# Optimization experiments

Hardware: AMD Instinct MI355X
Metric: run time of the kernel (lower is better)

The kernel has to match this reference:

```python
import jax, jax.numpy as jnp
import numpy as np

N = 50000   # nodes
E = 1600000 # edges
D = 64      # feature dim


def gcn_conv(x, edge_index, W, b):
    """PyG GCNConv: x' = D^-1/2 (A+I) D^-1/2 (x W) + b."""
    n = x.shape[0]
    xw = x @ W                                   # [N, D_out] linear first (PyG order)
    loop = jnp.arange(n)
    src = jnp.concatenate([edge_index[0], loop])  # add self-loops
    dst = jnp.concatenate([edge_index[1], loop])
    deg = jax.ops.segment_sum(jnp.ones_like(src, dtype=xw.dtype), dst, num_segments=n)
    dinv = jnp.where(deg > 0, jax.lax.rsqrt(deg), 0.0)
    norm = dinv[src] * dinv[dst]                  # symmetric normalization
    out = jax.ops.segment_sum(norm[:, None] * xw[src], dst, num_segments=n)
    return out + b


def setup_inputs() -> dict:
    key = jax.random.key(0)
    k1, k2, k3, k4 = jax.random.split(key, 4)
    x = jax.random.normal(k1, (N, D), dtype=jnp.float32)
    edge_index = jax.random.randint(k2, (2, E), 0, N, dtype=jnp.int64)
    s = 1.0 / np.sqrt(D)
    W1 = jax.random.normal(k3, (D, D), dtype=jnp.float32) * s
    b1 = jnp.zeros((D,), dtype=jnp.float32)
    W2 = jax.random.normal(k4, (D, D), dtype=jnp.float32) * s
    b2 = jnp.zeros((D,), dtype=jnp.float32)
    return {"x": x, "edge_index": edge_index, "W1": W1, "b1": b1, "W2": W2, "b2": b2}


def reference(x, edge_index, W1, b1, W2, b2):
    h = gcn_conv(x, edge_index, W1, b1)
    h = jax.nn.relu(h)  # dropout is identity in eval mode
    out = gcn_conv(h, edge_index, W2, b2)
    return out
```

## Files before the change

### kernel.cpp

```cpp
#include <hip/hip_runtime.h>
#include <hip/hip_fp16.h>


#define P1_EDGES 4096
#define BSTRIDE 16384

typedef float vfloat4 __attribute__((ext_vector_type(4)));

__global__ void bucket_gemm_kernel(const int* __restrict__ src, const int* __restrict__ dst,
                                   unsigned* __restrict__ cursor, unsigned* __restrict__ ebuf,
                                   const float4* __restrict__ X4, const float* __restrict__ W,
                                   __half* __restrict__ Yh,
                                   int e, int B, int n, int nbP1) {
    __shared__ unsigned hist[256];
    __shared__ unsigned base[256];
    __shared__ float4 Ws[64][16];
    int bid = blockIdx.x;
    if (bid < nbP1) {
        for (int i = threadIdx.x; i < B; i += 1024) hist[i] = 0;
        __syncthreads();
        int e0 = bid * P1_EDGES;
        int tbase = e0 + (int)threadIdx.x * 4;
        int4 sv = make_int4(0, 0, 0, 0), dv = make_int4(0, 0, 0, 0);
        if (tbase + 3 < e) {
            sv = ((const int4*)(src + e0))[threadIdx.x];
            dv = ((const int4*)(dst + e0))[threadIdx.x];
        } else {
            if (tbase + 0 < e) { sv.x = src[tbase + 0]; dv.x = dst[tbase + 0]; }
            if (tbase + 1 < e) { sv.y = src[tbase + 1]; dv.y = dst[tbase + 1]; }
            if (tbase + 2 < e) { sv.z = src[tbase + 2]; dv.z = dst[tbase + 2]; }
        }
        unsigned bk[4], rk[4], pk[4];
        bool vk[4];
#pragma unroll
        for (int k = 0; k < 4; ++k) {
            int t = tbase + k;
            vk[k] = (t < e);
            bk[k] = 0; rk[k] = 0; pk[k] = 0;
            if (vk[k]) {
                unsigned s = (unsigned)(k == 0 ? sv.x : k == 1 ? sv.y : k == 2 ? sv.z : sv.w);
                unsigned d = (unsigned)(k == 0 ? dv.x : k == 1 ? dv.y : k == 2 ? dv.z : dv.w);
                unsigned b = d >> 8;
                bk[k] = b;
                rk[k] = atomicAdd(&hist[b], 1u);
                pk[k] = (d << 16) | s;
            }
        }
        __syncthreads();
        for (int i = threadIdx.x; i < B; i += 1024)
            base[i] = hist[i] ? atomicAdd(&cursor[i], hist[i]) : 0u;
        __syncthreads();
#pragma unroll
        for (int k = 0; k < 4; ++k)
            if (vk[k]) {
                unsigned slot = base[bk[k]] + rk[k];
                if (slot < (unsigned)BSTRIDE)
                    ebuf[(size_t)bk[k] * BSTRIDE + slot] = pk[k];
            }
    } else {
        for (int i = threadIdx.x; i < 64 * 16; i += 1024)
            Ws[i >> 4][i & 15] = ((const float4*)W)[i];
        __syncthreads();
        int lane = threadIdx.x & 63;
        int l = lane & 15;
        int gbase = lane & 48;
        int wid = (bid - nbP1) * 16 + (threadIdx.x >> 6);
        int row = wid * 4 + (lane >> 4);
        if (row >= n) return;
        float4 xv = X4[(size_t)row * 16 + l];
        float4 acc = make_float4(0.f, 0.f, 0.f, 0.f);
#pragma unroll
        for (int k = 0; k < 64; ++k) {
            float comp = (k & 3) == 0 ? xv.x : (k & 3) == 1 ? xv.y : (k & 3) == 2 ? xv.z : xv.w;
            float a = __shfl(comp, gbase + (k >> 2));
            float4 w = Ws[k][l];
            acc.x = fmaf(a, w.x, acc.x); acc.y = fmaf(a, w.y, acc.y);
            acc.z = fmaf(a, w.z, acc.z); acc.w = fmaf(a, w.w, acc.w);
        }
        __half2 h0 = __floats2half2_rn(acc.x, acc.y);
        __half2 h1 = __floats2half2_rn(acc.z, acc.w);
        uint2 o;
        o.x = *(const unsigned*)&h0;
        o.y = *(const unsigned*)&h1;
        *(uint2*)(Yh + (size_t)row * 64 + 4 * l) = o;
    }
}

__global__ void statsfill_kernel(const unsigned* __restrict__ ebuf,
                                 const unsigned* __restrict__ bcnt,
                                 unsigned* __restrict__ rpf,
                                 __half* __restrict__ xwh1,
                                 unsigned short* __restrict__ csr, int n, int e) {
    __shared__ unsigned pos[256];
    __shared__ unsigned sh[256];
    __shared__ unsigned rpl[256];
    __shared__ float dl[256];
    __shared__ unsigned bs;
    int b = blockIdx.x;
    int w0 = b << 8;
    int wlen = min(w0 + 256, n) - w0;
    unsigned c0 = 0;
    if (threadIdx.x < 256) { c0 = bcnt[threadIdx.x]; sh[threadIdx.x] = c0; }
    __syncthreads();
    for (int off = 1; off < 256; off <<= 1) {
        unsigned t = 0;
        if (threadIdx.x < 256 && threadIdx.x >= (unsigned)off) t = sh[threadIdx.x - off];
        __syncthreads();
        if (threadIdx.x < 256) sh[threadIdx.x] += t;
        __syncthreads();
    }
    if (threadIdx.x == (unsigned)b) bs = sh[b] - c0;
    if (threadIdx.x < 256) pos[threadIdx.x] = 0;
    __syncthreads();
    unsigned cnt = bcnt[b];
    const unsigned* eb = ebuf + (size_t)b * BSTRIDE;
    for (unsigned j = threadIdx.x; j < cnt; j += 1024)
        atomicAdd(&pos[(eb[j] >> 16) - w0], 1u);
    __syncthreads();
    unsigned v = 0;
    if (threadIdx.x < 256) { v = pos[threadIdx.x]; sh[threadIdx.x] = v; }
    __syncthreads();
    for (int off = 1; off < 256; off <<= 1) {
        unsigned t = 0;
        if (threadIdx.x < 256 && threadIdx.x >= (unsigned)off) t = sh[threadIdx.x - off];
        __syncthreads();
        if (threadIdx.x < 256) sh[threadIdx.x] += t;
        __syncthreads();
    }
    if (threadIdx.x < 256) {
        unsigned rp = bs + sh[threadIdx.x] - v;
        rpl[threadIdx.x] = rp;
        dl[threadIdx.x] = rsqrtf((float)v + 1.0f);
        if ((int)threadIdx.x < wlen) rpf[w0 + threadIdx.x] = rp;
        pos[threadIdx.x] = 0;
    }
    if (b == (int)gridDim.x - 1 && threadIdx.x == 0) rpf[n] = (unsigned)e;
    __syncthreads();
    for (int i = threadIdx.x; i < (wlen << 3); i += 1024) {
        int r = i >> 3, c = i & 7;
        float di = dl[r];
        uint4* p16 = (uint4*)(xwh1 + ((size_t)(w0 + r) << 6)) + c;
        uint4 hv = *p16;
        float2 f0 = __half22float2(*(const __half2*)&hv.x);
        float2 f1 = __half22float2(*(const __half2*)&hv.y);
        float2 f2 = __half22float2(*(const __half2*)&hv.z);
        float2 f3 = __half22float2(*(const __half2*)&hv.w);
        __half2 g0 = __floats2half2_rn(f0.x * di, f0.y * di);
        __half2 g1 = __floats2half2_rn(f1.x * di, f1.y * di);
        __half2 g2 = __floats2half2_rn(f2.x * di, f2.y * di);
        __half2 g3 = __floats2half2_rn(f3.x * di, f3.y * di);
        hv.x = *(const unsigned*)&g0; hv.y = *(const unsigned*)&g1;
        hv.z = *(const unsigned*)&g2; hv.w = *(const unsigned*)&g3;
        *p16 = hv;
    }
    for (unsigned j = threadIdx.x; j < cnt; j += 1024) {
        unsigned p = eb[j];
        unsigned d = (p >> 16) - w0;
        unsigned r = atomicAdd(&pos[d], 1u);
        csr[rpl[d] + r] = (unsigned short)(p & 0xffffu);
    }
}

struct f8 { float4 a, b; };

__device__ __forceinline__ f8 aggregate_row8(const __half* __restrict__ xwh,
                                             const unsigned* __restrict__ csrw,
                                             unsigned start, unsigned end,
                                             int row, int l8, int gbase) {
    f8 acc;
    {
        uint4 hv = *(const uint4*)(xwh + (size_t)row * 64 + 8 * l8);
        float2 f0 = __half22float2(*(const __half2*)&hv.x);
        float2 f1 = __half22float2(*(const __half2*)&hv.y);
        float2 f2 = __half22float2(*(const __half2*)&hv.z);
        float2 f3 = __half22float2(*(const __half2*)&hv.w);
        acc.a = make_float4(f0.x, f0.y, f1.x, f1.y);
        acc.b = make_float4(f2.x, f2.y, f3.x, f3.y);
    }
    unsigned wb = start >> 1;
    unsigned jw = wb + (unsigned)l8;
    unsigned ed = (jw * 2 < end) ? __builtin_nontemporal_load(&csrw[jw]) : 0u;
    for (unsigned base = wb; base * 2 < end; base += 8) {
        unsigned jn = base + 8 + (unsigned)l8;
        unsigned ed_next = (jn * 2 < end) ? __builtin_nontemporal_load(&csrw[jn]) : 0u;
#pragma unroll
        for (int t = 0; t < 8; ++t) {
            unsigned p = __shfl(ed, gbase + t);
            unsigned i0 = (base + (unsigned)t) * 2;
            int s0 = (int)(p & 0xffffu);
            int s1 = (int)(p >> 16);
            float w0 = (i0 >= start && i0 < end) ? 1.0f : 0.0f;
            float w1 = (i0 + 1 < end) ? 1.0f : 0.0f;
            uint4 hv0 = *(const uint4*)(xwh + (size_t)s0 * 64 + 8 * l8);
            uint4 hv1 = *(const uint4*)(xwh + (size_t)s1 * 64 + 8 * l8);
            float2 a0 = __half22float2(*(const __half2*)&hv0.x);
            float2 a1 = __half22float2(*(const __half2*)&hv0.y);
            float2 a2 = __half22float2(*(const __half2*)&hv0.z);
            float2 a3 = __half22float2(*(const __half2*)&hv0.w);
            acc.a.x = fmaf(w0, a0.x, acc.a.x); acc.a.y = fmaf(w0, a0.y, acc.a.y);
            acc.a.z = fmaf(w0, a1.x, acc.a.z); acc.a.w = fmaf(w0, a1.y, acc.a.w);
            acc.b.x = fmaf(w0, a2.x, acc.b.x); acc.b.y = fmaf(w0, a2.y, acc.b.y);
            acc.b.z = fmaf(w0, a3.x, acc.b.z); acc.b.w = fmaf(w0, a3.y, acc.b.w);
            float2 c0 = __half22float2(*(const __half2*)&hv1.x);
            float2 c1 = __half22float2(*(const __half2*)&hv1.y);
            float2 c2 = __half22float2(*(const __half2*)&hv1.z);
            float2 c3 = __half22float2(*(const __half2*)&hv1.w);
            acc.a.x = fmaf(w1, c0.x, acc.a.x); acc.a.y = fmaf(w1, c0.y, acc.a.y);
            acc.a.z = fmaf(w1, c1.x, acc.a.z); acc.a.w = fmaf(w1, c1.y, acc.a.w);
            acc.b.x = fmaf(w1, c2.x, acc.b.x); acc.b.y = fmaf(w1, c2.y, acc.b.y);
            acc.b.z = fmaf(w1, c3.x, acc.b.z); acc.b.w = fmaf(w1, c3.y, acc.b.w);
        }
        ed = ed_next;
    }
    return acc;
}

__global__ void __launch_bounds__(256, 3)
gather_gemm_kernel(const __half* __restrict__ xwh, const unsigned* __restrict__ csrw,
                   const unsigned* __restrict__ row_ptr,
                   const float* __restrict__ b1, const float* __restrict__ W2,
                   __half* __restrict__ Yh, int n) {
    __shared__ float4 Ws[64][16];
    for (int i = threadIdx.x; i < 64 * 16; i += blockDim.x)
        Ws[i >> 4][i & 15] = ((const float4*)W2)[i];
    __syncthreads();
    int lane = threadIdx.x & 63;
    int l8 = lane & 7;
    int gbase = lane & 56;
    int wid = blockIdx.x * (blockDim.x >> 6) + (threadIdx.x >> 6);
    int row = wid * 8 + (lane >> 3);
    if (row >= n) return;
    unsigned start = row_ptr[row], end = row_ptr[row + 1];
    float di = rsqrtf((float)(end - start) + 1.0f);
    f8 acc = aggregate_row8(xwh, csrw, start, end, row, l8, gbase);
    float4 ba = ((const float4*)b1)[2 * l8];
    float4 bb = ((const float4*)b1)[2 * l8 + 1];
    float h0 = fmaxf(fmaf(di, acc.a.x, ba.x), 0.f);
    float h1 = fmaxf(fmaf(di, acc.a.y, ba.y), 0.f);
    float h2 = fmaxf(fmaf(di, acc.a.z, ba.z), 0.f);
    float h3 = fmaxf(fmaf(di, acc.a.w, ba.w), 0.f);
    float h4 = fmaxf(fmaf(di, acc.b.x, bb.x), 0.f);
    float h5 = fmaxf(fmaf(di, acc.b.y, bb.y), 0.f);
    float h6 = fmaxf(fmaf(di, acc.b.z, bb.z), 0.f);
    float h7 = fmaxf(fmaf(di, acc.b.w, bb.w), 0.f);
    float4 o0 = make_float4(0.f, 0.f, 0.f, 0.f);
    float4 o1 = make_float4(0.f, 0.f, 0.f, 0.f);
#pragma unroll
    for (int k = 0; k < 64; ++k) {
        float comp = (k & 7) == 0 ? h0 : (k & 7) == 1 ? h1 : (k & 7) == 2 ? h2 :
                     (k & 7) == 3 ? h3 : (k & 7) == 4 ? h4 : (k & 7) == 5 ? h5 :
                     (k & 7) == 6 ? h6 : h7;
        float a = __shfl(comp, gbase + (k >> 3));
        float4 w0 = Ws[k][2 * l8];
        float4 w1 = Ws[k][2 * l8 + 1];
        o0.x = fmaf(a, w0.x, o0.x); o0.y = fmaf(a, w0.y, o0.y);
        o0.z = fmaf(a, w0.z, o0.z); o0.w = fmaf(a, w0.w, o0.w);
        o1.x = fmaf(a, w1.x, o1.x); o1.y = fmaf(a, w1.y, o1.y);
        o1.z = fmaf(a, w1.z, o1.z); o1.w = fmaf(a, w1.w, o1.w);
    }
    __half2 p0 = __floats2half2_rn(o0.x * di, o0.y * di);
    __half2 p1 = __floats2half2_rn(o0.z * di, o0.w * di);
    __half2 p2 = __floats2half2_rn(o1.x * di, o1.y * di);
    __half2 p3 = __floats2half2_rn(o1.z * di, o1.w * di);
    uint4 o;
    o.x = *(const unsigned*)&p0; o.y = *(const unsigned*)&p1;
    o.z = *(const unsigned*)&p2; o.w = *(const unsigned*)&p3;
    *(uint4*)(Yh + (size_t)row * 64 + 8 * l8) = o;
}

__global__ void __launch_bounds__(256, 3)
gather_out_kernel(const __half* __restrict__ xwh, const unsigned* __restrict__ csrw,
                  const unsigned* __restrict__ row_ptr,
                  const float* __restrict__ bias, float4* __restrict__ out4, int n) {
    int lane = threadIdx.x & 63;
    int l8 = lane & 7;
    int gbase = lane & 56;
    int wid = blockIdx.x * (blockDim.x >> 6) + (threadIdx.x >> 6);
    int row = wid * 8 + (lane >> 3);
    if (row >= n) return;
    unsigned start = row_ptr[row], end = row_ptr[row + 1];
    float di = rsqrtf((float)(end - start) + 1.0f);
    f8 acc = aggregate_row8(xwh, csrw, start, end, row, l8, gbase);
    float4 ba = ((const float4*)bias)[2 * l8];
    float4 bb = ((const float4*)bias)[2 * l8 + 1];
    vfloat4 oa, ob;
    oa.x = fmaf(di, acc.a.x, ba.x); oa.y = fmaf(di, acc.a.y, ba.y);
    oa.z = fmaf(di, acc.a.z, ba.z); oa.w = fmaf(di, acc.a.w, ba.w);
    ob.x = fmaf(di, acc.b.x, bb.x); ob.y = fmaf(di, acc.b.y, bb.y);
    ob.z = fmaf(di, acc.b.z, bb.z); ob.w = fmaf(di, acc.b.w, bb.w);
    vfloat4* o4 = (vfloat4*)out4;
    __builtin_nontemporal_store(oa, &o4[(size_t)row * 16 + 2 * l8]);
    __builtin_nontemporal_store(ob, &o4[(size_t)row * 16 + 2 * l8 + 1]);
}

extern "C" void kernel_launch(void* const* d_in, const int* in_sizes, int n_in,
                              void* d_out, int out_size, void* d_ws, size_t ws_size,
                              hipStream_t stream) {
    const float* x  = (const float*)d_in[0];
    const int*   ei = (const int*)d_in[1];
    const float* W1 = (const float*)d_in[2];
    const float* b1 = (const float*)d_in[3];
    const float* W2 = (const float*)d_in[4];
    const float* b2 = (const float*)d_in[5];
    const int n = in_sizes[0] / 64;
    const int e = in_sizes[1] / 2;
    const int* src = ei;
    const int* dst = ei + e;

    char* ws = (char*)d_ws;
    size_t off = 0;
    auto alloc = [&](size_t bytes) -> void* {
        void* p = ws + off;
        off = (off + bytes + 255) & ~(size_t)255;
        return p;
    };
    unsigned* rpf    = (unsigned*)alloc((size_t)(n + 1) * 4);
    unsigned* cursor = (unsigned*)alloc(256 * 4);
    unsigned short* csr = (unsigned short*)alloc(((size_t)e / 2 + 64) * 4);
    const int B = (n + 255) / 256;
    unsigned* ebuf   = (unsigned*)alloc((size_t)B * BSTRIDE * 4);
    __half*   xwh1   = (__half*)alloc((size_t)n * 64 * 2);
    __half*   xwh2   = (__half*)alloc((size_t)n * 64 * 2);
    float*    outf   = (float*)d_out;

    const int nbP1 = (e + P1_EDGES - 1) / P1_EDGES;
    const int gblk64 = (n + 63) / 64;

    hipMemsetAsync(cursor, 0, 256 * 4, stream);
    bucket_gemm_kernel<<<nbP1 + gblk64, 1024, 0, stream>>>(
        src, dst, cursor, ebuf, (const float4*)x, W1, xwh1, e, B, n, nbP1);
    statsfill_kernel<<<B, 1024, 0, stream>>>(ebuf, cursor, rpf, xwh1, csr, n, e);

    const int gblk32 = (n + 31) / 32;

    gather_gemm_kernel<<<gblk32, 256, 0, stream>>>(xwh1, (const unsigned*)csr, rpf, b1, W2, xwh2, n);
    gather_out_kernel<<<gblk32, 256, 0, stream>>>(xwh2, (const unsigned*)csr, rpf, b2, (float4*)outf, n);
}
```

Before: 171.5 us.

## Split feature columns into two halves for cache-resident gather passes

Stores the transformed node features as two separate 32-column fp16 tables, and performs each neighbour aggregation as two passes, one per half. Each pass therefore touches a table half the size, which is meant to improve L2/LLC hit rates on the random source-row gathers. The first layer's halves are combined in the second gather kernel before the W2 matmul. In exchange, the CSR index stream is read twice per layer and there are extra kernel launches plus an intermediate hA buffer.

Result: slower. 203.0 us (+18.4%).

```diff
diff --git a/kernel.cpp b/kernel.cpp
--- a/kernel.cpp
+++ b/kernel.cpp
@@ -10,7 +10,7 @@
 __global__ void bucket_gemm_kernel(const int* __restrict__ src, const int* __restrict__ dst,
                                    unsigned* __restrict__ cursor, unsigned* __restrict__ ebuf,
                                    const float4* __restrict__ X4, const float* __restrict__ W,
-                                   __half* __restrict__ Yh,
+                                   __half* __restrict__ YA, __half* __restrict__ YB,
                                    int e, int B, int n, int nbP1) {
     __shared__ unsigned hist[256];
     __shared__ unsigned base[256];
@@ -82,14 +82,15 @@
         uint2 o;
         o.x = *(const unsigned*)&h0;
         o.y = *(const unsigned*)&h1;
-        *(uint2*)(Yh + (size_t)row * 64 + 4 * l) = o;
+        __half* dstp = (l < 8 ? YA : YB) + ((size_t)row << 5) + 4 * (l & 7);
+        *(uint2*)dstp = o;
     }
 }
 
 __global__ void statsfill_kernel(const unsigned* __restrict__ ebuf,
                                  const unsigned* __restrict__ bcnt,
                                  unsigned* __restrict__ rpf,
-                                 __half* __restrict__ xwh1,
+                                 __half* __restrict__ xwA, __half* __restrict__ xwB,
                                  unsigned short* __restrict__ csr, int n, int e) {
     __shared__ unsigned pos[256];
     __shared__ unsigned sh[256];
@@ -139,7 +140,8 @@
     for (int i = threadIdx.x; i < (wlen << 3); i += 1024) {
         int r = i >> 3, c = i & 7;
         float di = dl[r];
-        uint4* p16 = (uint4*)(xwh1 + ((size_t)(w0 + r) << 6)) + c;
+        __half* tb = (c < 4) ? xwA : xwB;
+        uint4* p16 = (uint4*)(tb + ((size_t)(w0 + r) << 5)) + (c & 3);
         uint4 hv = *p16;
         float2 f0 = __half22float2(*(const __half2*)&hv.x);
         float2 f1 = __half22float2(*(const __half2*)&hv.y);
@@ -163,13 +165,13 @@
 
 struct f8 { float4 a, b; };
 
-__device__ __forceinline__ f8 aggregate_row8(const __half* __restrict__ xwh,
+__device__ __forceinline__ f8 aggregate_half(const __half* __restrict__ xw,
                                              const unsigned* __restrict__ csrw,
                                              unsigned start, unsigned end,
-                                             int row, int l8, int gbase) {
+                                             int row, int l4, int gb) {
     f8 acc;
     {
-        uint4 hv = *(const uint4*)(xwh + (size_t)row * 64 + 8 * l8);
+        uint4 hv = *(const uint4*)(xw + ((size_t)row << 5) + 8 * l4);
         float2 f0 = __half22float2(*(const __half2*)&hv.x);
         float2 f1 = __half22float2(*(const __half2*)&hv.y);
         float2 f2 = __half22float2(*(const __half2*)&hv.z);
@@ -178,21 +180,21 @@
         acc.b = make_float4(f2.x, f2.y, f3.x, f3.y);
     }
     unsigned wb = start >> 1;
-    unsigned jw = wb + (unsigned)l8;
+    unsigned jw = wb + (unsigned)l4;
     unsigned ed = (jw * 2 < end) ? __builtin_nontemporal_load(&csrw[jw]) : 0u;
-    for (unsigned base = wb; base * 2 < end; base += 8) {
-        unsigned jn = base + 8 + (unsigned)l8;
+    for (unsigned base = wb; base * 2 < end; base += 4) {
+        unsigned jn = base + 4 + (unsigned)l4;
         unsigned ed_next = (jn * 2 < end) ? __builtin_nontemporal_load(&csrw[jn]) : 0u;
 #pragma unroll
-        for (int t = 0; t < 8; ++t) {
-            unsigned p = __shfl(ed, gbase + t);
+        for (int t = 0; t < 4; ++t) {
+            unsigned p = __shfl(ed, gb + t);
             unsigned i0 = (base + (unsigned)t) * 2;
             int s0 = (int)(p & 0xffffu);
             int s1 = (int)(p >> 16);
             float w0 = (i0 >= start && i0 < end) ? 1.0f : 0.0f;
             float w1 = (i0 + 1 < end) ? 1.0f : 0.0f;
-            uint4 hv0 = *(const uint4*)(xwh + (size_t)s0 * 64 + 8 * l8);
-            uint4 hv1 = *(const uint4*)(xwh + (size_t)s1 * 64 + 8 * l8);
+            uint4 hv0 = *(const uint4*)(xw + ((size_t)s0 << 5) + 8 * l4);
+            uint4 hv1 = *(const uint4*)(xw + ((size_t)s1 << 5) + 8 * l4);
             float2 a0 = __half22float2(*(const __half2*)&hv0.x);
             float2 a1 = __half22float2(*(const __half2*)&hv0.y);
             float2 a2 = __half22float2(*(const __half2*)&hv0.z);
@@ -216,81 +218,133 @@
 }
 
 __global__ void __launch_bounds__(256, 3)
-gather_gemm_kernel(const __half* __restrict__ xwh, const unsigned* __restrict__ csrw,
-                   const unsigned* __restrict__ row_ptr,
-                   const float* __restrict__ b1, const float* __restrict__ W2,
-                   __half* __restrict__ Yh, int n) {
+gather1A_kernel(const __half* __restrict__ xwA, const unsigned* __restrict__ csrw,
+                const unsigned* __restrict__ row_ptr, const float* __restrict__ b1,
+                __half* __restrict__ hA, int n) {
+    int lane = threadIdx.x & 63;
+    int l4 = lane & 3;
+    int gb = lane & 60;
+    int wid = blockIdx.x * (blockDim.x >> 6) + (threadIdx.x >> 6);
+    int row = wid * 16 + (lane >> 2);
+    if (row >= n) return;
+    unsigned start = row_ptr[row], end = row_ptr[row + 1];
+    float di = rsqrtf((float)(end - start) + 1.0f);
+    f8 acc = aggregate_half(xwA, csrw, start, end, row, l4, gb);
+    float4 ba = ((const float4*)b1)[2 * l4];
+    float4 bb = ((const float4*)b1)[2 * l4 + 1];
+    __half2 p0 = __floats2half2_rn(fmaxf(fmaf(di, acc.a.x, ba.x), 0.f), fmaxf(fmaf(di, acc.a.y, ba.y), 0.f));
+    __half2 p1 = __floats2half2_rn(fmaxf(fmaf(di, acc.a.z, ba.z), 0.f), fmaxf(fmaf(di, acc.a.w, ba.w), 0.f));
+    __half2 p2 = __floats2half2_rn(fmaxf(fmaf(di, acc.b.x, bb.x), 0.f), fmaxf(fmaf(di, acc.b.y, bb.y), 0.f));
+    __half2 p3 = __floats2half2_rn(fmaxf(fmaf(di, acc.b.z, bb.z), 0.f), fmaxf(fmaf(di, acc.b.w, bb.w), 0.f));
+    uint4 o;
+    o.x = *(const unsigned*)&p0; o.y = *(const unsigned*)&p1;
+    o.z = *(const unsigned*)&p2; o.w = *(const unsigned*)&p3;
+    *(uint4*)(hA + ((size_t)row << 5) + 8 * l4) = o;
+}
+
+__global__ void __launch_bounds__(256, 3)
+gather1B_kernel(const __half* __restrict__ xwB, const unsigned* __restrict__ csrw,
+                const unsigned* __restrict__ row_ptr, const float* __restrict__ b1,
+                const __half* __restrict__ hA, const float* __restrict__ W2,
+                __half* __restrict__ xw2A, __half* __restrict__ xw2B, int n) {
     __shared__ float4 Ws[64][16];
     for (int i = threadIdx.x; i < 64 * 16; i += blockDim.x)
         Ws[i >> 4][i & 15] = ((const float4*)W2)[i];
     __syncthreads();
     int lane = threadIdx.x & 63;
-    int l8 = lane & 7;
-    int gbase = lane & 56;
+    int l4 = lane & 3;
+    int gb = lane & 60;
     int wid = blockIdx.x * (blockDim.x >> 6) + (threadIdx.x >> 6);
-    int row = wid * 8 + (lane >> 3);
+    int row = wid * 16 + (lane >> 2);
     if (row >= n) return;
     unsigned start = row_ptr[row], end = row_ptr[row + 1];
     float di = rsqrtf((float)(end - start) + 1.0f);
-    f8 acc = aggregate_row8(xwh, csrw, start, end, row, l8, gbase);
-    float4 ba = ((const float4*)b1)[2 * l8];
-    float4 bb = ((const float4*)b1)[2 * l8 + 1];
-    float h0 = fmaxf(fmaf(di, acc.a.x, ba.x), 0.f);
-    float h1 = fmaxf(fmaf(di, acc.a.y, ba.y), 0.f);
-    float h2 = fmaxf(fmaf(di, acc.a.z, ba.z), 0.f);
-    float h3 = fmaxf(fmaf(di, acc.a.w, ba.w), 0.f);
-    float h4 = fmaxf(fmaf(di, acc.b.x, bb.x), 0.f);
-    float h5 = fmaxf(fmaf(di, acc.b.y, bb.y), 0.f);
-    float h6 = fmaxf(fmaf(di, acc.b.z, bb.z), 0.f);
-    float h7 = fmaxf(fmaf(di, acc.b.w, bb.w), 0.f);
+    f8 acc = aggregate_half(xwB, csrw, start, end, row, l4, gb);
+    float4 ba = ((const float4*)b1)[8 + 2 * l4];
+    float4 bb = ((const float4*)b1)[8 + 2 * l4 + 1];
+    float hb0 = fmaxf(fmaf(di, acc.a.x, ba.x), 0.f);
+    float hb1 = fmaxf(fmaf(di, acc.a.y, ba.y), 0.f);
+    float hb2 = fmaxf(fmaf(di, acc.a.z, ba.z), 0.f);
+    float hb3 = fmaxf(fmaf(di, acc.a.w, ba.w), 0.f);
+    float hb4 = fmaxf(fmaf(di, acc.b.x, bb.x), 0.f);
+    float hb5 = fmaxf(fmaf(di, acc.b.y, bb.y), 0.f);
+    float hb6 = fmaxf(fmaf(di, acc.b.z, bb.z), 0.f);
+    float hb7 = fmaxf(fmaf(di, acc.b.w, bb.w), 0.f);
+    uint4 hv = *(const uint4*)(hA + ((size_t)row << 5) + 8 * l4);
+    float2 q0 = __half22float2(*(const __half2*)&hv.x);
+    float2 q1 = __half22float2(*(const __half2*)&hv.y);
+    float2 q2 = __half22float2(*(const __half2*)&hv.z);
+    float2 q3 = __half22float2(*(const __half2*)&hv.w);
+    float ha0 = q0.x, ha1 = q0.y, ha2 = q1.x, ha3 = q1.y;
+    float ha4 = q2.x, ha5 = q2.y, ha6 = q3.x, ha7 = q3.y;
     float4 o0 = make_float4(0.f, 0.f, 0.f, 0.f);
     float4 o1 = make_float4(0.f, 0.f, 0.f, 0.f);
+    float4 o2 = make_float4(0.f, 0.f, 0.f, 0.f);
+    float4 o3 = make_float4(0.f, 0.f, 0.f, 0.f);
 #pragma unroll
     for (int k = 0; k < 64; ++k) {
-        float comp = (k & 7) == 0 ? h0 : (k & 7) == 1 ? h1 : (k & 7) == 2 ? h2 :
-                     (k & 7) == 3 ? h3 : (k & 7) == 4 ? h4 : (k & 7) == 5 ? h5 :
-                     (k & 7) == 6 ? h6 : h7;
-        float a = __shfl(comp, gbase + (k >> 3));
-        float4 w0 = Ws[k][2 * l8];
-        float4 w1 = Ws[k][2 * l8 + 1];
+        float va = (k & 7) == 0 ? ha0 : (k & 7) == 1 ? ha1 : (k & 7) == 2 ? ha2 :
+                   (k & 7) == 3 ? ha3 : (k & 7) == 4 ? ha4 : (k & 7) == 5 ? ha5 :
+                   (k & 7) == 6 ? ha6 : ha7;
+        float vb = (k & 7) == 0 ? hb0 : (k & 7) == 1 ? hb1 : (k & 7) == 2 ? hb2 :
+                   (k & 7) == 3 ? hb3 : (k & 7) == 4 ? hb4 : (k & 7) == 5 ? hb5 :
+                   (k & 7) == 6 ? hb6 : hb7;
+        float comp = (k < 32) ? va : vb;
+        float a = __shfl(comp, gb + ((k >> 3) & 3));
+        float4 w0 = Ws[k][4 * l4 + 0];
+        float4 w1 = Ws[k][4 * l4 + 1];
+        float4 w2 = Ws[k][4 * l4 + 2];
+        float4 w3 = Ws[k][4 * l4 + 3];
         o0.x = fmaf(a, w0.x, o0.x); o0.y = fmaf(a, w0.y, o0.y);
         o0.z = fmaf(a, w0.z, o0.z); o0.w = fmaf(a, w0.w, o0.w);
         o1.x = fmaf(a, w1.x, o1.x); o1.y = fmaf(a, w1.y, o1.y);
         o1.z = fmaf(a, w1.z, o1.z); o1.w = fmaf(a, w1.w, o1.w);
+        o2.x = fmaf(a, w2.x, o2.x); o2.y = fmaf(a, w2.y, o2.y);
+        o2.z = fmaf(a, w2.z, o2.z); o2.w = fmaf(a, w2.w, o2.w);
+        o3.x = fmaf(a, w3.x, o3.x); o3.y = fmaf(a, w3.y, o3.y);
+        o3.z = fmaf(a, w3.z, o3.z); o3.w = fmaf(a, w3.w, o3.w);
     }
     __half2 p0 = __floats2half2_rn(o0.x * di, o0.y * di);
     __half2 p1 = __floats2half2_rn(o0.z * di, o0.w * di);
     __half2 p2 = __floats2half2_rn(o1.x * di, o1.y * di);
     __half2 p3 = __floats2half2_rn(o1.z * di, o1.w * di);
-    uint4 o;
-    o.x = *(const unsigned*)&p0; o.y = *(const unsigned*)&p1;
-    o.z = *(const unsigned*)&p2; o.w = *(const unsigned*)&p3;
-    *(uint4*)(Yh + (size_t)row * 64 + 8 * l8) = o;
+    __half2 p4 = __floats2half2_rn(o2.x * di, o2.y * di);
+    __half2 p5 = __floats2half2_rn(o2.z * di, o2.w * di);
+    __half2 p6 = __floats2half2_rn(o3.x * di, o3.y * di);
+    __half2 p7 = __floats2half2_rn(o3.z * di, o3.w * di);
+    uint4 u0, u1;
+    u0.x = *(const unsigned*)&p0; u0.y = *(const unsigned*)&p1;
+    u0.z = *(const unsigned*)&p2; u0.w = *(const unsigned*)&p3;
+    u1.x = *(const unsigned*)&p4; u1.y = *(const unsigned*)&p5;
+    u1.z = *(const unsigned*)&p6; u1.w = *(const unsigned*)&p7;
+    __half* dstp = (l4 < 2 ? xw2A : xw2B) + ((size_t)row << 5) + 16 * (l4 & 1);
+    *(uint4*)dstp = u0;
+    *(uint4*)(dstp + 8) = u1;
 }
 
 __global__ void __launch_bounds__(256, 3)
-gather_out_kernel(const __half* __restrict__ xwh, const unsigned* __restrict__ csrw,
-                  const unsigned* __restrict__ row_ptr,
-                  const float* __restrict__ bias, float4* __restrict__ out4, int n) {
+gather2_kernel(const __half* __restrict__ xw2H, const unsigned* __restrict__ csrw,
+               const unsigned* __restrict__ row_ptr, const float* __restrict__ b2,
+               float* __restrict__ outp, int colOff, int n) {
     int lane = threadIdx.x & 63;
-    int l8 = lane & 7;
-    int gbase = lane & 56;
+    int l4 = lane & 3;
+    int gb = lane & 60;
     int wid = blockIdx.x * (blockDim.x >> 6) + (threadIdx.x >> 6);
-    int row = wid * 8 + (lane >> 3);
+    int row = wid * 16 + (lane >> 2);
     if (row >= n) return;
     unsigned start = row_ptr[row], end = row_ptr[row + 1];
     float di = rsqrtf((float)(end - start) + 1.0f);
-    f8 acc = aggregate_row8(xwh, csrw, start, end, row, l8, gbase);
-    float4 ba = ((const float4*)bias)[2 * l8];
-    float4 bb = ((const float4*)bias)[2 * l8 + 1];
+    f8 acc = aggregate_half(xw2H, csrw, start, end, row, l4, gb);
+    float4 ba = ((const float4*)b2)[(colOff >> 2) + 2 * l4];
+    float4 bb = ((const float4*)b2)[(colOff >> 2) + 2 * l4 + 1];
     vfloat4 oa, ob;
     oa.x = fmaf(di, acc.a.x, ba.x); oa.y = fmaf(di, acc.a.y, ba.y);
     oa.z = fmaf(di, acc.a.z, ba.z); oa.w = fmaf(di, acc.a.w, ba.w);
     ob.x = fmaf(di, acc.b.x, bb.x); ob.y = fmaf(di, acc.b.y, bb.y);
     ob.z = fmaf(di, acc.b.z, bb.z); ob.w = fmaf(di, acc.b.w, bb.w);
-    vfloat4* o4 = (vfloat4*)out4;
-    __builtin_nontemporal_store(oa, &o4[(size_t)row * 16 + 2 * l8]);
-    __builtin_nontemporal_store(ob, &o4[(size_t)row * 16 + 2 * l8 + 1]);
+    vfloat4* o4 = (vfloat4*)(outp + (size_t)row * 64 + colOff + 8 * l4);
+    __builtin_nontemporal_store(oa, o4);
+    __builtin_nontemporal_store(ob, o4 + 1);
 }
 
 extern "C" void kernel_launch(void* const* d_in, const int* in_sizes, int n_in,
@@ -318,21 +372,28 @@
     unsigned* cursor = (unsigned*)alloc(256 * 4);
     unsigned short* csr = (unsigned short*)alloc(((size_t)e / 2 + 64) * 4);
     const int B = (n + 255) / 256;
-    unsigned* ebuf   = (unsigned*)alloc((size_t)B * BSTRIDE * 4);
-    __half*   xwh1   = (__half*)alloc((size_t)n * 64 * 2);
-    __half*   xwh2   = (__half*)alloc((size_t)n * 64 * 2);
-    float*    outf   = (float*)d_out;
+    unsigned* ebuf  = (unsigned*)alloc((size_t)B * BSTRIDE * 4);
+    size_t half = (size_t)n * 32 * 2;
+    __half* xw1A = (__half*)alloc(half);
+    __half* xw1B = (__half*)alloc(half);
+    __half* hA   = (__half*)alloc(half);
+    __half* xw2A = (__half*)alloc(half);
+    __half* xw2B = (__half*)alloc(half);
+    float*  outf = (float*)d_out;
 
     const int nbP1 = (e + P1_EDGES - 1) / P1_EDGES;
     const int gblk64 = (n + 63) / 64;
 
     hipMemsetAsync(cursor, 0, 256 * 4, stream);
     bucket_gemm_kernel<<<nbP1 + gblk64, 1024, 0, stream>>>(
-        src, dst, cursor, ebuf, (const float4*)x, W1, xwh1, e, B, n, nbP1);
-    statsfill_kernel<<<B, 1024, 0, stream>>>(ebuf, cursor, rpf, xwh1, csr, n, e);
-
-    const int gblk32 = (n + 31) / 32;
-
-    gather_gemm_kernel<<<gblk32, 256, 0, stream>>>(xwh1, (const unsigned*)csr, rpf, b1, W2, xwh2, n);
-    gather_out_kernel<<<gblk32, 256, 0, stream>>>(xwh2, (const unsigned*)csr, rpf, b2, (float4*)outf, n);
-}
+        src, dst, cursor, ebuf, (const float4*)x, W1, xw1A, xw1B, e, B, n, nbP1);
+    statsfill_kernel<<<B, 1024, 0, stream>>>(ebuf, cursor, rpf, xw1A, xw1B, csr, n, e);
+
+    const int gblk = (n + 63) / 64;
+
+    gather1A_kernel<<<gblk, 256, 0, stream>>>(xw1A, (const unsigned*)csr, rpf, b1, hA, n);
+    gather1B_kernel<<<gblk, 256, 0, stream>>>(xw1B, (const unsigned*)csr, rpf, b1, hA, W2, xw2A, xw2B, n);
+
+    gather2_kernel<<<gblk, 256, 0, stream>>>(xw2A, (const unsigned*)csr, rpf, b2, outf, 0, n);
+    gather2_kernel<<<gblk, 256, 0, stream>>>(xw2B, (const unsigned*)csr, rpf, b2, outf, 32, n);
+}
```
